# Kernel tuning notes

Hardware: AMD Instinct MI355X
Metric: run time of the kernel (lower is better)

The kernel has to match this reference:

```python
import jax, jax.numpy as jnp
import numpy as np

ALPHA = 32.0
RANK = 16


def setup_inputs() -> dict:
    key = jax.random.key(0)
    ks = jax.random.split(key, 6)
    d_in, d_out, r = 4096, 4096, RANK
    x = jax.random.normal(ks[0], (4, 2048, d_in), dtype=jnp.float32)
    W = jax.random.normal(ks[1], (d_out, d_in), dtype=jnp.float32) * (1.0 / np.sqrt(d_in))
    bias = jax.random.normal(ks[2], (d_out,), dtype=jnp.float32) * 0.02
    B_lora = jax.random.normal(ks[3], (d_out, r), dtype=jnp.float32) * (1.0 / np.sqrt(r))
    A_lora = jax.random.normal(ks[4], (r, d_in), dtype=jnp.float32) * (1.0 / np.sqrt(d_in))
    delta_bias = jax.random.normal(ks[5], (d_out,), dtype=jnp.float32) * 0.02
    return {"x": x, "W": W, "bias": bias, "B_lora": B_lora, "A_lora": A_lora, "delta_bias": delta_bias}


def reference(x, W, bias, B_lora, A_lora, delta_bias):
    # LoRALinear.forward with adapter_enabled=True:
    # y = x @ (W + (alpha/rank) * B @ A).T + bias + (alpha/rank) * delta_bias
    # Expressed as base GEMM + two small low-rank GEMMs (same math, no
    # [out, in] delta-weight materialization).
    scale = ALPHA / RANK
    base = jnp.einsum('bsi,oi->bso', x, W)              # [B,S,out]
    xa = jnp.einsum('bsi,ri->bsr', x, A_lora)           # [B,S,r]
    delta = jnp.einsum('bsr,or->bso', xa, B_lora)       # [B,S,out]
    return base + scale * delta + bias + scale * delta_bias
```

## Files before the change

kernel.cpp:

```cpp
#include <hip/hip_runtime.h>
#include <stdint.h>

#define M_DIM 8192
#define N_DIM 4096
#define K_DIM 4096

typedef __attribute__((ext_vector_type(4))) float f32x4;
typedef __attribute__((ext_vector_type(8))) __bf16 bf16x8;

__device__ __forceinline__ unsigned short f2bf(float f) {
  unsigned int u = __builtin_bit_cast(unsigned int, f);
  u += 0x7FFFu + ((u >> 16) & 1u);
  return (unsigned short)(u >> 16);
}

__device__ __forceinline__ void load16_lds(const void* g, void* l) {
  __builtin_amdgcn_global_load_lds(
      (__attribute__((address_space(1))) void*)g,
      (__attribute__((address_space(3))) void*)l,
      16, 0, 0);
}

#define WAITVM(N) asm volatile("s_waitcnt vmcnt(" #N ")" ::: "memory")
#define BARRIER() asm volatile("s_barrier" ::: "memory")

__global__ __launch_bounds__(256) void cvt_x_kernel(const float* __restrict__ x,
                                                    unsigned short* __restrict__ xb) {
  const int n8 = (M_DIM * K_DIM) / 8;
  int i = blockIdx.x * blockDim.x + threadIdx.x;
  const int stride = gridDim.x * blockDim.x;
  for (; i < n8; i += stride) {
    const float4* p = (const float4*)x + (size_t)i * 2;
    const float4 a = p[0];
    const float4 b = p[1];
    uint4 o;
    o.x = (unsigned)f2bf(a.x) | ((unsigned)f2bf(a.y) << 16);
    o.y = (unsigned)f2bf(a.z) | ((unsigned)f2bf(a.w) << 16);
    o.z = (unsigned)f2bf(b.x) | ((unsigned)f2bf(b.y) << 16);
    o.w = (unsigned)f2bf(b.z) | ((unsigned)f2bf(b.w) << 16);
    ((uint4*)xb)[i] = o;
  }
}

__global__ __launch_bounds__(256) void build_wb_kernel(const float* __restrict__ W,
                                                       const float* __restrict__ B_lora,
                                                       const float* __restrict__ A_lora,
                                                       unsigned short* __restrict__ wb) {
  __shared__ float As[64][17];
  __shared__ float Bs[64][17];
  const int t = threadIdx.x;
  const int i0 = blockIdx.x * 64;
  const int o0 = blockIdx.y * 64;
  {
    const int c = t & 63;
    #pragma unroll
    for (int rr = (t >> 6); rr < 16; rr += 4)
      As[c][rr] = A_lora[rr * K_DIM + i0 + c];
    const int r2 = t & 15;
    #pragma unroll
    for (int oo = (t >> 4); oo < 64; oo += 16)
      Bs[oo][r2] = B_lora[(o0 + oo) * 16 + r2];
  }
  __syncthreads();
  const int ci = t & 63;
  const int og = t >> 6;
  float areg[16];
  #pragma unroll
  for (int r = 0; r < 16; ++r) areg[r] = As[ci][r];
  const int i = i0 + ci;
  #pragma unroll 4
  for (int j = 0; j < 16; ++j) {
    const int ol = og * 16 + j;
    float d = 0.f;
    #pragma unroll
    for (int r = 0; r < 16; ++r) d += Bs[ol][r] * areg[r];
    const size_t idx = (size_t)(o0 + ol) * K_DIM + i;
    wb[idx] = f2bf(W[idx] + 2.0f * d);
  }
}

__global__ __launch_bounds__(512, 2) void gemm_kernel(const unsigned short* __restrict__ xb,
                                                      const unsigned short* __restrict__ wb,
                                                      const float* __restrict__ bias,
                                                      const float* __restrict__ dbias,
                                                      float* __restrict__ out) {
  constexpr int BK = 64;
  constexpr int NT = K_DIM / BK;
  __shared__ char As[65536];
  __shared__ char Bs[65536];

  const int t = threadIdx.x;
  const int w = t >> 6, l = t & 63;
  const int wr = w >> 2, wc = w & 3;
  constexpr int NBN = N_DIM / 256;
  constexpr int NWG = (M_DIM / 256) * NBN;
  int bid = (int)blockIdx.x;
  bid = (bid & 7) * (NWG >> 3) + (bid >> 3);
  const int m0 = (bid / NBN) * 256;
  const int n0 = (bid % NBN) * 256;

  const int trow = t >> 3;
  const int scol = ((t & 7) ^ (trow & 7)) * 8;
  const int rowoffA[4] = {0, 128, 64, 192};
  const int ldsoffA[4] = {0, 16384, 8192, 24576};
  const unsigned short* gAp[4];
  #pragma unroll
  for (int j = 0; j < 4; ++j)
    gAp[j] = xb + (size_t)(m0 + rowoffA[j] + trow) * K_DIM + scol;
  const unsigned short* gBp[4];
  #pragma unroll
  for (int j = 0; j < 4; ++j) {
    const int rp = j * 64 + trow;
    const int gr = (rp & 31) + ((rp >> 5) & 3) * 64 + (rp >> 7) * 32;
    gBp[j] = wb + (size_t)(n0 + gr) * K_DIM + scol;
  }
  const int wlds = w * 1024;

  const int swz = (l & 7) << 4;
  const int rdk = (l >> 4) * 16;
  const int rdA = (wr * 128 + (l & 15)) * 128;
  const int rdB = (wc * 32 + (l & 15)) * 128;

  f32x4 acc[8][4];
  #pragma unroll
  for (int i = 0; i < 8; ++i)
    #pragma unroll
    for (int j = 0; j < 4; ++j) acc[i][j] = f32x4{0.f, 0.f, 0.f, 0.f};
  bf16x8 afA[4][2], afB[4][2];
  bf16x8 bfA[2][2], bfB[2][2];

#define STAGE_A(CUR, SLOT, KT) \
  load16_lds(gAp[SLOT] + (KT), As + (CUR) * 32768 + ldsoffA[SLOT] + wlds)
#define STAGE_B(CUR, SLOT, KT) \
  load16_lds(gBp[SLOT] + (KT), Bs + (CUR) * 32768 + (SLOT) * 8192 + wlds)

#define READ_A(CUR, MH, DST)                                                  \
  {                                                                           \
    const char* base_ = As + (CUR) * 32768 + rdA + (MH) * 8192;               \
    _Pragma("unroll") for (int mf_ = 0; mf_ < 4; ++mf_)                       \
      _Pragma("unroll") for (int ks_ = 0; ks_ < 2; ++ks_)                     \
        DST[mf_][ks_] = *(const bf16x8*)(base_ + mf_ * 2048 +                 \
                                         ((ks_ * 64 + rdk) ^ swz));           \
  }
#define READ_B(CUR, NH, DST)                                                  \
  {                                                                           \
    const char* base_ = Bs + (CUR) * 32768 + rdB + (NH) * 16384;              \
    _Pragma("unroll") for (int nf_ = 0; nf_ < 2; ++nf_)                       \
      _Pragma("unroll") for (int ks_ = 0; ks_ < 2; ++ks_)                     \
        DST[nf_][ks_] = *(const bf16x8*)(base_ + nf_ * 2048 +                 \
                                         ((ks_ * 64 + rdk) ^ swz));           \
  }
#define QUAD(MH, NH, AFR, BFR)                                                \
  {                                                                           \
    __builtin_amdgcn_s_setprio(1);                                            \
    _Pragma("unroll") for (int mf_ = 0; mf_ < 4; ++mf_)                       \
      _Pragma("unroll") for (int nf_ = 0; nf_ < 2; ++nf_)                     \
        _Pragma("unroll") for (int ks_ = 0; ks_ < 2; ++ks_)                   \
          acc[(MH) * 4 + mf_][(NH) * 2 + nf_] =                               \
              __builtin_amdgcn_mfma_f32_16x16x32_bf16(                        \
                  AFR[mf_][ks_], BFR[nf_][ks_],                               \
                  acc[(MH) * 4 + mf_][(NH) * 2 + nf_], 0, 0, 0);              \
    __builtin_amdgcn_s_setprio(0);                                            \
  }

  STAGE_A(0, 0, 0); STAGE_A(0, 1, 0);
  STAGE_B(0, 0, 0); STAGE_B(0, 1, 0);
  STAGE_B(0, 2, 0); STAGE_B(0, 3, 0);
  STAGE_A(0, 2, 0); STAGE_A(0, 3, 0);
  WAITVM(2);
  BARRIER();
  READ_A(0, 0, afA); READ_B(0, 0, bfA);

  int cur = 0;
  for (int kt = 0; kt < NT - 1; ++kt) {
    const int kn = (kt + 1) * BK;
    const int nxt = cur ^ 1;
    READ_B(cur, 1, bfB);
    STAGE_A(nxt, 0, kn); STAGE_A(nxt, 1, kn);
    BARRIER(); QUAD(0, 0, afA, bfA); WAITVM(2); BARRIER();
    READ_A(cur, 1, afB);
    STAGE_B(nxt, 0, kn); STAGE_B(nxt, 1, kn);
    STAGE_B(nxt, 2, kn); STAGE_B(nxt, 3, kn);
    BARRIER(); QUAD(0, 1, afA, bfB); WAITVM(4); BARRIER();
    QUAD(1, 1, afB, bfB);
    READ_A(nxt, 0, afA);
    WAITVM(2); BARRIER();
    STAGE_A(nxt, 2, kn); STAGE_A(nxt, 3, kn);
    BARRIER(); QUAD(1, 0, afB, bfA);
    READ_B(nxt, 0, bfA);
    WAITVM(2); BARRIER();
    cur = nxt;
  }
  READ_B(cur, 1, bfB);
  BARRIER(); QUAD(0, 0, afA, bfA); WAITVM(0); BARRIER();
  READ_A(cur, 1, afB);
  QUAD(0, 1, afA, bfB);
  QUAD(1, 1, afB, bfB);
  QUAD(1, 0, afB, bfA);

  float bv[4];
  #pragma unroll
  for (int nf = 0; nf < 4; ++nf) {
    const int c = n0 + wc * 64 + nf * 16 + (l & 15);
    bv[nf] = bias[c] + 2.0f * dbias[c];
  }
  #pragma unroll
  for (int mf = 0; mf < 8; ++mf) {
    const int r0 = m0 + wr * 128 + mf * 16 + ((l >> 4) << 2);
    #pragma unroll
    for (int nf = 0; nf < 4; ++nf) {
      const int c = n0 + wc * 64 + nf * 16 + (l & 15);
      const f32x4 v = acc[mf][nf];
      #pragma unroll
      for (int j = 0; j < 4; ++j)
        out[(size_t)(r0 + j) * N_DIM + c] = v[j] + bv[nf];
    }
  }
#undef STAGE_A
#undef STAGE_B
#undef READ_A
#undef READ_B
#undef QUAD
}

__global__ __launch_bounds__(256) void xa_kernel(const float* __restrict__ x,
                                                 const float* __restrict__ A_lora,
                                                 float* __restrict__ xa) {
  const int m = blockIdx.x;
  const int t = threadIdx.x;
  float acc[16];
  #pragma unroll
  for (int r = 0; r < 16; ++r) acc[r] = 0.f;
  const float* xr = x + (size_t)m * K_DIM;
  for (int k = t; k < K_DIM; k += 256) {
    const float xv = xr[k];
    #pragma unroll
    for (int r = 0; r < 16; ++r) acc[r] += xv * A_lora[r * K_DIM + k];
  }
  __shared__ float red[16][4];
  #pragma unroll
  for (int r = 0; r < 16; ++r) {
    float v = acc[r];
    for (int off = 32; off > 0; off >>= 1) v += __shfl_down(v, off, 64);
    if ((t & 63) == 0) red[r][t >> 6] = v;
  }
  __syncthreads();
  if (t < 16) xa[(size_t)m * 16 + t] = red[t][0] + red[t][1] + red[t][2] + red[t][3];
}

__global__ __launch_bounds__(256) void fgemm_kernel(const float* __restrict__ x,
                                                    const float* __restrict__ W,
                                                    const float* __restrict__ bias,
                                                    const float* __restrict__ B_lora,
                                                    const float* __restrict__ dbias,
                                                    const float* __restrict__ xa,
                                                    float* __restrict__ out) {
  __shared__ float As[64][17];
  __shared__ float Ws[64][17];
  const int t = threadIdx.x;
  const int m0 = (blockIdx.x >> 6) * 64;
  const int n0 = (blockIdx.x & 63) * 64;
  const int tx = t & 15, ty = t >> 4;
  float c[4][4] = {};
  for (int kt = 0; kt < K_DIM; kt += 16) {
    #pragma unroll
    for (int e = 0; e < 4; ++e) {
      const int q = t + e * 256;
      const int r = q >> 4, k = q & 15;
      As[r][k] = x[(size_t)(m0 + r) * K_DIM + kt + k];
      Ws[r][k] = W[(size_t)(n0 + r) * K_DIM + kt + k];
    }
    __syncthreads();
    #pragma unroll
    for (int k = 0; k < 16; ++k) {
      float a[4], b[4];
      #pragma unroll
      for (int ii = 0; ii < 4; ++ii) a[ii] = As[ty * 4 + ii][k];
      #pragma unroll
      for (int jj = 0; jj < 4; ++jj) b[jj] = Ws[tx * 4 + jj][k];
      #pragma unroll
      for (int ii = 0; ii < 4; ++ii)
        #pragma unroll
        for (int jj = 0; jj < 4; ++jj) c[ii][jj] += a[ii] * b[jj];
    }
    __syncthreads();
  }
  #pragma unroll
  for (int ii = 0; ii < 4; ++ii) {
    const int row = m0 + ty * 4 + ii;
    #pragma unroll
    for (int jj = 0; jj < 4; ++jj) {
      const int col = n0 + tx * 4 + jj;
      float d = 0.f;
      #pragma unroll
      for (int r = 0; r < 16; ++r) d += xa[(size_t)row * 16 + r] * B_lora[col * 16 + r];
      out[(size_t)row * N_DIM + col] = c[ii][jj] + 2.0f * d + bias[col] + 2.0f * dbias[col];
    }
  }
}

extern "C" void kernel_launch(void* const* d_in, const int* in_sizes, int n_in,
                              void* d_out, int out_size, void* d_ws, size_t ws_size,
                              hipStream_t stream) {
  const float* x = (const float*)d_in[0];
  const float* W = (const float*)d_in[1];
  const float* bias = (const float*)d_in[2];
  const float* B_lora = (const float*)d_in[3];
  const float* A_lora = (const float*)d_in[4];
  const float* dbias = (const float*)d_in[5];
  float* out = (float*)d_out;

  const size_t NEED = (size_t)M_DIM * K_DIM * 2 + (size_t)N_DIM * K_DIM * 2;
  if (ws_size >= NEED) {
    unsigned short* xb = (unsigned short*)d_ws;
    unsigned short* wb = xb + (size_t)M_DIM * K_DIM;
    cvt_x_kernel<<<2048, 256, 0, stream>>>(x, xb);
    build_wb_kernel<<<dim3(64, 64), 256, 0, stream>>>(W, B_lora, A_lora, wb);
    gemm_kernel<<<(M_DIM / 256) * (N_DIM / 256), 512, 0, stream>>>(xb, wb, bias, dbias, out);
  } else {
    float* xa = (float*)d_ws;
    xa_kernel<<<M_DIM, 256, 0, stream>>>(x, A_lora, xa);
    fgemm_kernel<<<(M_DIM / 64) * (N_DIM / 64), 256, 0, stream>>>(x, W, bias, B_lora, dbias, xa, out);
  }
}
```

Measured before the change: 545.1 us.

## Restructure GEMM main loop to prefetch two K-tiles ahead with reordered quadrants

The GEMM main loop is rescheduled so global-to-LDS staging runs two K-tiles ahead instead of one. The quadrant order changes, explicit lgkmcnt waits are added before each MFMA quadrant, and the barrier uses the compiler builtin. The aim is to hide more global-load latency behind MFMA work and cut stalls at vmcnt waits. The cost is more complex buffer reuse across the two LDS buffers, which risks hazards if the barrier and wait placement is wrong.

```diff
diff --git a/kernel.cpp b/kernel.cpp
--- a/kernel.cpp
+++ b/kernel.cpp
@@ -22,7 +22,8 @@
 }
 
 #define WAITVM(N) asm volatile("s_waitcnt vmcnt(" #N ")" ::: "memory")
-#define BARRIER() asm volatile("s_barrier" ::: "memory")
+#define LGKMH(N)  asm volatile("s_waitcnt lgkmcnt(" #N ")" ::: "memory")
+#define BARRIER() __builtin_amdgcn_s_barrier()
 
 __global__ __launch_bounds__(256) void cvt_x_kernel(const float* __restrict__ x,
                                                     unsigned short* __restrict__ xb) {
@@ -165,38 +166,52 @@
 
   STAGE_A(0, 0, 0); STAGE_A(0, 1, 0);
   STAGE_B(0, 0, 0); STAGE_B(0, 1, 0);
+  STAGE_A(0, 2, 0); STAGE_A(0, 3, 0);
   STAGE_B(0, 2, 0); STAGE_B(0, 3, 0);
-  STAGE_A(0, 2, 0); STAGE_A(0, 3, 0);
-  WAITVM(2);
+  STAGE_A(1, 0, BK); STAGE_A(1, 1, BK);
+  STAGE_B(1, 0, BK); STAGE_B(1, 1, BK);
+  STAGE_A(1, 2, BK); STAGE_A(1, 3, BK);
+  WAITVM(6);
   BARRIER();
-  READ_A(0, 0, afA); READ_B(0, 0, bfA);
-
-  int cur = 0;
-  for (int kt = 0; kt < NT - 1; ++kt) {
-    const int kn = (kt + 1) * BK;
-    const int nxt = cur ^ 1;
-    READ_B(cur, 1, bfB);
-    STAGE_A(nxt, 0, kn); STAGE_A(nxt, 1, kn);
-    BARRIER(); QUAD(0, 0, afA, bfA); WAITVM(2); BARRIER();
-    READ_A(cur, 1, afB);
-    STAGE_B(nxt, 0, kn); STAGE_B(nxt, 1, kn);
-    STAGE_B(nxt, 2, kn); STAGE_B(nxt, 3, kn);
-    BARRIER(); QUAD(0, 1, afA, bfB); WAITVM(4); BARRIER();
-    QUAD(1, 1, afB, bfB);
-    READ_A(nxt, 0, afA);
-    WAITVM(2); BARRIER();
-    STAGE_A(nxt, 2, kn); STAGE_A(nxt, 3, kn);
-    BARRIER(); QUAD(1, 0, afB, bfA);
-    READ_B(nxt, 0, bfA);
-    WAITVM(2); BARRIER();
-    cur = nxt;
-  }
-  READ_B(cur, 1, bfB);
-  BARRIER(); QUAD(0, 0, afA, bfA); WAITVM(0); BARRIER();
-  READ_A(cur, 1, afB);
+
+  for (int kt = 0; kt < NT - 2; ++kt) {
+    const int b = kt & 1;
+    const int k1 = (kt + 1) * BK;
+    const int k2 = (kt + 2) * BK;
+    READ_A(b, 0, afA); READ_B(b, 0, bfA);
+    STAGE_B(b ^ 1, 2, k1); STAGE_B(b ^ 1, 3, k1);
+    LGKMH(8);
+    BARRIER(); LGKMH(0); QUAD(0, 0, afA, bfA); BARRIER();
+    READ_A(b, 1, afB);
+    STAGE_A(b, 0, k2); STAGE_A(b, 1, k2);
+    BARRIER(); LGKMH(0); QUAD(1, 0, afB, bfA); BARRIER();
+    READ_B(b, 1, bfB);
+    STAGE_B(b, 0, k2); STAGE_B(b, 1, k2);
+    BARRIER(); LGKMH(0); QUAD(1, 1, afB, bfB); BARRIER();
+    STAGE_A(b, 2, k2); STAGE_A(b, 3, k2);
+    WAITVM(6);
+    BARRIER(); QUAD(0, 1, afA, bfB); BARRIER();
+  }
+  {
+    const int k1 = (NT - 1) * BK;
+    READ_A(0, 0, afA); READ_B(0, 0, bfA);
+    STAGE_B(1, 2, k1); STAGE_B(1, 3, k1);
+    LGKMH(8);
+    BARRIER(); LGKMH(0); QUAD(0, 0, afA, bfA); BARRIER();
+    READ_A(0, 1, afB);
+    BARRIER(); LGKMH(0); QUAD(1, 0, afB, bfA); BARRIER();
+    READ_B(0, 1, bfB);
+    BARRIER(); LGKMH(0); QUAD(1, 1, afB, bfB); BARRIER();
+    WAITVM(0);
+    BARRIER(); QUAD(0, 1, afA, bfB); BARRIER();
+  }
+  READ_A(1, 0, afA); READ_B(1, 0, bfA);
+  QUAD(0, 0, afA, bfA);
+  READ_A(1, 1, afB);
+  QUAD(1, 0, afB, bfA);
+  READ_B(1, 1, bfB);
+  QUAD(1, 1, afB, bfB);
   QUAD(0, 1, afA, bfB);
-  QUAD(1, 1, afB, bfB);
-  QUAD(1, 0, afB, bfA);
 
   float bv[4];
   #pragma unroll
```

Result: no change. 535.3 us (-1.8%).
